# Optimization experiments

Measured on AMD Instinct MI355X. Metric: run time of the kernel, lower is better.

Reference implementation:

```python
import jax, jax.numpy as jnp
import numpy as np

B, T, DIM = 2, 2048, 2048
N_HEAD, N_GROUP = 16, 4
KV_HEAD = N_HEAD // N_GROUP
HEAD_DIM = DIM // N_HEAD


def setup_inputs() -> dict:
    key = jax.random.key(0)
    ks = jax.random.split(key, 7)
    x = jax.random.normal(ks[0], (B, T, DIM), dtype=jnp.float32)
    # rotary tables: last dim = head_dim // 2 (interleaved real/imag pairs)
    pos = jnp.arange(T, dtype=jnp.float32)[:, None]
    inv_freq = 1.0 / (10000.0 ** (jnp.arange(0, HEAD_DIM, 2, dtype=jnp.float32) / HEAD_DIM))
    angles = pos * inv_freq[None, :]  # [T, HEAD_DIM//2]
    freqs_cos = jnp.cos(angles)
    freqs_sin = jnp.sin(angles)
    scale = 0.02
    wq = jax.random.normal(ks[1], (DIM, N_HEAD * HEAD_DIM), dtype=jnp.float32) * scale
    wk = jax.random.normal(ks[2], (DIM, KV_HEAD * HEAD_DIM), dtype=jnp.float32) * scale
    wv = jax.random.normal(ks[3], (DIM, KV_HEAD * HEAD_DIM), dtype=jnp.float32) * scale
    wo = jax.random.normal(ks[4], (N_HEAD * HEAD_DIM, DIM), dtype=jnp.float32) * scale
    return {"x": x, "freqs_cos": freqs_cos, "freqs_sin": freqs_sin,
            "wq": wq, "wk": wk, "wv": wv, "wo": wo}


def _apply_rope(t, cos, sin):
    # t: [B, T, H, D]; interleaved pairs (..., -1, 2) as in torch reference
    tr = t.reshape(*t.shape[:-1], -1, 2)
    r, i = tr[..., 0], tr[..., 1]
    c = cos[None, :, None, :]  # [1, T, 1, D//2]
    s = sin[None, :, None, :]
    out = jnp.stack([r * c - i * s, r * s + i * c], axis=-1)
    return out.reshape(t.shape)


def reference(x, freqs_cos, freqs_sin, wq, wk, wv, wo):
    Bx, Tx, C = x.shape
    xq = (x @ wq).reshape(Bx, Tx, N_HEAD, HEAD_DIM)
    xk = (x @ wk).reshape(Bx, Tx, KV_HEAD, HEAD_DIM)
    xv = (x @ wv).reshape(Bx, Tx, KV_HEAD, HEAD_DIM)
    xq = _apply_rope(xq, freqs_cos, freqs_sin)
    xk = _apply_rope(xk, freqs_cos, freqs_sin)
    # repeat_kv: each kv head repeated n_group times consecutively
    xk = jnp.repeat(xk, N_GROUP, axis=2)  # [B, T, N_HEAD, D]
    xv = jnp.repeat(xv, N_GROUP, axis=2)
    scale = HEAD_DIM ** -0.5
    att = jnp.einsum('bqhd,bkhd->bhqk', xq, xk) * scale
    causal = jnp.tril(jnp.ones((Tx, Tx), dtype=bool))
    att = jnp.where(causal[None, None], att, -jnp.inf)
    att = jax.nn.softmax(att, axis=-1)
    out = jnp.einsum('bhqk,bkhd->bqhd', att, xv).reshape(Bx, Tx, N_HEAD * HEAD_DIM)
    return out @ wo
```

## Files before the change

kernel.cpp:

```cpp
#include <hip/hip_runtime.h>

#define TB 2
#define TT 2048
#define TDIM 2048
#define NHEADS 16
#define KVHEADS 4
#define HD 128

typedef unsigned short u16;
typedef unsigned int u32;
typedef __attribute__((ext_vector_type(8))) short short8;
typedef __attribute__((ext_vector_type(4))) float float4_t;

__device__ __forceinline__ float b2f(u16 u) {
    union { u32 i; float f; } v; v.i = ((u32)u) << 16; return v.f;
}
__device__ __forceinline__ u16 f2b(float f) {
    union { float f; u32 i; } v; v.f = f;
    u32 r = (v.i + 0x7FFFu + ((v.i >> 16) & 1u)) >> 16;
    return (u16)r;
}
__device__ __forceinline__ u32 fbits(float f) {
    union { float f; u32 i; } v; v.f = f; return v.i;
}

__device__ __forceinline__ void gl_lds16(const void* g, void* l) {
    __builtin_amdgcn_global_load_lds((const __attribute__((address_space(1))) void*)g,
                                     (__attribute__((address_space(3))) void*)l, 16, 0, 0);
}

template <bool F32OUT, bool ROPE>
__global__ __launch_bounds__(256, 3)
void gemm_bt(const u16* __restrict__ A, const u16* __restrict__ BT,
             void* __restrict__ Cv, int M, int N, int K,
             const float* __restrict__ fc, const float* __restrict__ fs) {
    __shared__ __align__(16) u16 As[128 * 64];
    __shared__ __align__(16) u16 Bs[128 * 64];
    const int tid  = threadIdx.x;
    const int wave = tid >> 6, lane = tid & 63;
    const int quad = lane >> 4, l16 = lane & 15;
    const int wm = wave >> 1, wn = wave & 1;
    const int row0 = blockIdx.y * 128, col0 = blockIdx.x * 128;

    float4_t acc[4][4];
#pragma unroll
    for (int i = 0; i < 4; i++)
#pragma unroll
        for (int j = 0; j < 4; j++) acc[i][j] = (float4_t){0.f, 0.f, 0.f, 0.f};

    for (int kk = 0; kk < K; kk += 64) {
        __syncthreads();
#pragma unroll
        for (int i = 0; i < 4; i++) {
            int n = i * 256 + wave * 64 + lane;
            int r = n >> 3, c = (n & 7) ^ (r & 7);
            gl_lds16(A  + (size_t)(row0 + r) * K + kk + c * 8, &As[(i * 256 + wave * 64) * 8]);
            gl_lds16(BT + (size_t)(col0 + r) * K + kk + c * 8, &Bs[(i * 256 + wave * 64) * 8]);
        }
        __syncthreads();
#pragma unroll
        for (int ks = 0; ks < 2; ks++) {
            short8 af[4], bf[4];
#pragma unroll
            for (int mt = 0; mt < 4; mt++) {
                int m = wm * 64 + mt * 16 + l16;
                af[mt] = *(const short8*)&As[(m * 8 + ((ks * 4 + quad) ^ (l16 & 7))) * 8];
            }
#pragma unroll
            for (int nt = 0; nt < 4; nt++) {
                int n = wn * 64 + nt * 16 + l16;
                bf[nt] = *(const short8*)&Bs[(n * 8 + ((ks * 4 + quad) ^ (l16 & 7))) * 8];
            }
#pragma unroll
            for (int mt = 0; mt < 4; mt++)
#pragma unroll
                for (int nt = 0; nt < 4; nt++)
                    acc[mt][nt] = __builtin_amdgcn_mfma_f32_16x16x32_bf16(
                        af[mt], bf[nt], acc[mt][nt], 0, 0, 0);
        }
    }
    const bool do_rope = ROPE && (col0 < 2560);
#pragma unroll
    for (int mt = 0; mt < 4; mt++)
#pragma unroll
        for (int nt = 0; nt < 4; nt++)
#pragma unroll
            for (int r = 0; r < 4; r++) {
                int row = row0 + wm * 64 + mt * 16 + quad * 4 + r;
                int col = col0 + wn * 64 + nt * 16 + l16;
                float v = acc[mt][nt][r];
                if (ROPE && do_rope) {
                    float other = __shfl_xor(v, 1, 64);
                    int t = row & (TT - 1);
                    int i0 = (col & (HD - 1)) >> 1;
                    float c = fc[t * 64 + i0], s = fs[t * 64 + i0];
                    v = (col & 1) ? fmaf(v, c, other * s) : fmaf(v, c, -other * s);
                }
                if (F32OUT)
                    ((float*)Cv)[(size_t)row * N + col] = v;
                else
                    ((u16*)Cv)[(size_t)row * N + col] = f2b(v);
            }
}

template <bool F32OUT>
__global__ __launch_bounds__(512, 4)
void gemm_bt8w(const u16* __restrict__ A, const u16* __restrict__ BT,
               void* __restrict__ Cv, int M, int N, int K) {
    __shared__ __align__(16) u16 As[128 * 64];
    __shared__ __align__(16) u16 Bs[128 * 64];
    const int tid  = threadIdx.x;
    const int w    = tid >> 6, lane = tid & 63;
    const int quad = lane >> 4, l16 = lane & 15;
    const int wm = w >> 1, wn = w & 1;
    const int row0 = blockIdx.y * 128, col0 = blockIdx.x * 128;

    float4_t acc[2][4];
#pragma unroll
    for (int i = 0; i < 2; i++)
#pragma unroll
        for (int j = 0; j < 4; j++) acc[i][j] = (float4_t){0.f, 0.f, 0.f, 0.f};

    for (int kk = 0; kk < K; kk += 64) {
        __syncthreads();
#pragma unroll
        for (int j = 0; j < 2; j++) {
            int n = j * 512 + w * 64 + lane;
            int r = n >> 3, c = (n & 7) ^ (r & 7);
            gl_lds16(A  + (size_t)(row0 + r) * K + kk + c * 8, &As[(j * 512 + w * 64) * 8]);
            gl_lds16(BT + (size_t)(col0 + r) * K + kk + c * 8, &Bs[(j * 512 + w * 64) * 8]);
        }
        __syncthreads();
#pragma unroll
        for (int ks = 0; ks < 2; ks++) {
            short8 af[2], bf[4];
#pragma unroll
            for (int mt = 0; mt < 2; mt++) {
                int m = wm * 32 + mt * 16 + l16;
                af[mt] = *(const short8*)&As[(m * 8 + ((ks * 4 + quad) ^ (l16 & 7))) * 8];
            }
#pragma unroll
            for (int nt = 0; nt < 4; nt++) {
                int n = wn * 64 + nt * 16 + l16;
                bf[nt] = *(const short8*)&Bs[(n * 8 + ((ks * 4 + quad) ^ (l16 & 7))) * 8];
            }
#pragma unroll
            for (int mt = 0; mt < 2; mt++)
#pragma unroll
                for (int nt = 0; nt < 4; nt++)
                    acc[mt][nt] = __builtin_amdgcn_mfma_f32_16x16x32_bf16(
                        af[mt], bf[nt], acc[mt][nt], 0, 0, 0);
        }
    }
#pragma unroll
    for (int mt = 0; mt < 2; mt++)
#pragma unroll
        for (int nt = 0; nt < 4; nt++)
#pragma unroll
            for (int r = 0; r < 4; r++) {
                int row = row0 + wm * 32 + mt * 16 + quad * 4 + r;
                int col = col0 + wn * 64 + nt * 16 + l16;
                float v = acc[mt][nt][r];
                if (F32OUT)
                    ((float*)Cv)[(size_t)row * N + col] = v;
                else
                    ((u16*)Cv)[(size_t)row * N + col] = f2b(v);
            }
}

__global__ void prep(const float* __restrict__ x, u16* __restrict__ xb,
                     const float* __restrict__ wq, const float* __restrict__ wk,
                     const float* __restrict__ wv, const float* __restrict__ wo,
                     u16* __restrict__ WT, u16* __restrict__ woT) {
    const int bid = blockIdx.x;
    if (bid < 8192) {
        size_t i = ((size_t)bid * 256 + threadIdx.x) * 4;
        float4 v = *(const float4*)(x + i);
        ushort4 o;
        o.x = f2b(v.x); o.y = f2b(v.y); o.z = f2b(v.z); o.w = f2b(v.w);
        *(ushort4*)(xb + i) = o;
        return;
    }
    const int rem = bid - 8192;
    const int bx = rem % 160;
    const int by = rem / 160;
    const float* in; u16* out; int cols, cx;
    if (bx < 64)      { in = wq; out = WT;                         cols = 2048; cx = bx; }
    else if (bx < 80) { in = wk; out = WT + (size_t)2048 * 2048;   cols = 512;  cx = bx - 64; }
    else if (bx < 96) { in = wv; out = WT + (size_t)2560 * 2048;   cols = 512;  cx = bx - 80; }
    else              { in = wo; out = woT;                        cols = 2048; cx = bx - 96; }
    const int rows = 2048;
    __shared__ u16 tile[32][72];
    const int c0 = cx * 32, r0 = by * 64;
    const int tx = threadIdx.x & 31, ty = threadIdx.x >> 5;
#pragma unroll
    for (int i = 0; i < 8; i++) {
        int r = ty * 8 + i;
        tile[tx][r] = f2b(in[(size_t)(r0 + r) * cols + c0 + tx]);
    }
    __syncthreads();
    const int c = threadIdx.x >> 3, rc = threadIdx.x & 7;
    *(short8*)&out[(size_t)(c0 + c) * rows + r0 + rc * 8] =
        *(const short8*)&tile[c][rc * 8];
}

__global__ void transpose_v(const u16* __restrict__ QKV, u16* __restrict__ Vt) {
    int z = blockIdx.z, b = z >> 2, kv = z & 3;
    const u16* in = QKV + (size_t)b * TT * 3072 + 2560 + kv * HD;
    u16* out = Vt + (size_t)z * HD * TT;
    __shared__ u16 tile[32][72];
    const int t0 = blockIdx.x * 64, d0 = blockIdx.y * 32;
    const int tx = threadIdx.x & 31, ty = threadIdx.x >> 5;
#pragma unroll
    for (int i = 0; i < 8; i++) {
        int r = ty * 8 + i;
        tile[tx][r] = in[(size_t)(t0 + r) * 3072 + d0 + tx];
    }
    __syncthreads();
    const int c = threadIdx.x >> 3, rc = threadIdx.x & 7;
    *(short8*)&out[(size_t)(d0 + c) * TT + t0 + rc * 8] =
        *(const short8*)&tile[c][rc * 8];
}

#define PSTR 72
__global__ __launch_bounds__(256, 3)
void attn(const u16* __restrict__ QKV, const u16* __restrict__ Vt,
          u16* __restrict__ O) {
    const int bid = blockIdx.x;
    const int qb  = 31 - (bid >> 5);
    const int y   = bid & 31;
    const int b   = y >> 4;
    const int h   = y & 15;
    const int kvh = h >> 2;
    const int tid = threadIdx.x, w = tid >> 6, lane = tid & 63;
    const int quad = lane >> 4, l16 = lane & 15;

    __shared__ __align__(16) u16 Ks[64 * 128];
    __shared__ __align__(16) u16 Vs[128 * 64];
    __shared__ __align__(16) u16 Ps[4][16 * PSTR];

    const u16* Kbase = QKV + (size_t)b * TT * 3072 + 2048 + kvh * HD;
    const u16* Vbase = Vt + (size_t)(b * 4 + kvh) * HD * TT;
    const float Cl = 0.12753102474f;

    auto stageK = [&](int kt) {
#pragma unroll
        for (int i = 0; i < 4; i++) {
            int n = i * 256 + w * 64 + lane;
            int r = n >> 4, c = (n & 15) ^ (r & 15);
            gl_lds16(Kbase + (size_t)(kt * 64 + r) * 3072 + c * 8,
                     &Ks[(i * 256 + w * 64) * 8]);
        }
    };
    auto stageV = [&](int kt) {
#pragma unroll
        for (int i = 0; i < 4; i++) {
            int n = i * 256 + w * 64 + lane;
            int d = n >> 3, c = (n & 7) ^ (d & 7);
            gl_lds16(Vbase + (size_t)d * TT + kt * 64 + c * 8,
                     &Vs[(i * 256 + w * 64) * 8]);
        }
    };

    stageK(0);

    short8 qf[4];
    {
        const u16* Qrow = QKV + ((size_t)b * TT + qb * 64 + w * 16 + l16) * 3072
                          + h * HD;
#pragma unroll
        for (int ks = 0; ks < 4; ks++)
            qf[ks] = *(const short8*)(Qrow + ks * 32 + quad * 8);
    }

    float4_t o[8];
#pragma unroll
    for (int i = 0; i < 8; i++) o[i] = (float4_t){0.f, 0.f, 0.f, 0.f};
    float mi = -1e30f, li = 0.f;
    const int qg = qb * 64 + w * 16 + l16;

    for (int kt = 0; kt <= qb; kt++) {
        __syncthreads();
        stageV(kt);

        float4_t st[4];
#pragma unroll
        for (int nt = 0; nt < 4; nt++) st[nt] = (float4_t){0.f, 0.f, 0.f, 0.f};
#pragma unroll
        for (int ks = 0; ks < 4; ks++) {
            short8 af[4];
#pragma unroll
            for (int nt = 0; nt < 4; nt++)
                af[nt] = *(const short8*)&Ks[((nt * 16 + l16) * 16 +
                                             ((ks * 4 + quad) ^ l16)) * 8];
            __builtin_amdgcn_s_setprio(1);
#pragma unroll
            for (int nt = 0; nt < 4; nt++)
                st[nt] = __builtin_amdgcn_mfma_f32_16x16x32_bf16(
                    af[nt], qf[ks], st[nt], 0, 0, 0);
            __builtin_amdgcn_s_setprio(0);
        }

        if (kt == qb) {
#pragma unroll
            for (int nt = 0; nt < 4; nt++)
#pragma unroll
                for (int r = 0; r < 4; r++) {
                    int key = kt * 64 + nt * 16 + quad * 4 + r;
                    if (key > qg) st[nt][r] = -3e38f;
                }
        }
        float pm = -3e38f;
#pragma unroll
        for (int nt = 0; nt < 4; nt++)
#pragma unroll
            for (int r = 0; r < 4; r++) pm = fmaxf(pm, st[nt][r]);
        pm = fmaxf(pm, __shfl_xor(pm, 16, 64));
        pm = fmaxf(pm, __shfl_xor(pm, 32, 64));
        const bool need = !__all(pm - mi <= 62.7f);
        float alpha_v = 1.f;
        if (need) {
            float mnew = fmaxf(mi, pm);
            alpha_v = __builtin_amdgcn_exp2f((mi - mnew) * Cl);
            mi = mnew;
        }
        const float mC = mi * Cl;
        float rs = 0.f;
#pragma unroll
        for (int nt = 0; nt < 4; nt++)
#pragma unroll
            for (int r = 0; r < 4; r++) {
                float e = __builtin_amdgcn_exp2f(fmaf(st[nt][r], Cl, -mC));
                st[nt][r] = e;
                rs += e;
            }
        rs += __shfl_xor(rs, 16, 64);
        rs += __shfl_xor(rs, 32, 64);
        li = li * alpha_v + rs;

#pragma unroll
        for (int nt = 0; nt < 4; nt++) {
            uint2 pk;
            pk.x = __builtin_amdgcn_perm(fbits(st[nt][1]), fbits(st[nt][0]), 0x07060302u);
            pk.y = __builtin_amdgcn_perm(fbits(st[nt][3]), fbits(st[nt][2]), 0x07060302u);
            *(uint2*)&Ps[w][l16 * PSTR + nt * 16 + quad * 4] = pk;
        }
        if (need) {
            float a_o[4];
#pragma unroll
            for (int r = 0; r < 4; r++) a_o[r] = __shfl(alpha_v, quad * 4 + r, 64);
#pragma unroll
            for (int n2 = 0; n2 < 8; n2++)
#pragma unroll
                for (int r = 0; r < 4; r++) o[n2][r] *= a_o[r];
        }

        __syncthreads();
        if (kt < qb) stageK(kt + 1);

#pragma unroll
        for (int ks2 = 0; ks2 < 2; ks2++) {
            short8 ap = *(const short8*)&Ps[w][l16 * PSTR + ks2 * 32 + quad * 8];
            __builtin_amdgcn_s_setprio(1);
#pragma unroll
            for (int n2 = 0; n2 < 8; n2++) {
                short8 bv = *(const short8*)&Vs[((n2 * 16 + l16) * 8 +
                                                ((ks2 * 4 + quad) ^ (l16 & 7))) * 8];
                o[n2] = __builtin_amdgcn_mfma_f32_16x16x32_bf16(ap, bv, o[n2], 0, 0, 0);
            }
            __builtin_amdgcn_s_setprio(0);
        }
    }

    float linv[4];
#pragma unroll
    for (int r = 0; r < 4; r++) linv[r] = 1.0f / __shfl(li, quad * 4 + r, 64);
    u16* Ob2 = O + ((size_t)b * TT + qb * 64 + w * 16) * TDIM + h * HD;
#pragma unroll
    for (int n2 = 0; n2 < 8; n2++)
#pragma unroll
        for (int r = 0; r < 4; r++)
            Ob2[(size_t)(quad * 4 + r) * TDIM + n2 * 16 + l16] =
                f2b(o[n2][r] * linv[r]);
}

extern "C" void kernel_launch(void* const* d_in, const int* in_sizes, int n_in,
                              void* d_out, int out_size, void* d_ws, size_t ws_size,
                              hipStream_t stream) {
    const float* x  = (const float*)d_in[0];
    const float* fc = (const float*)d_in[1];
    const float* fs = (const float*)d_in[2];
    const float* wq = (const float*)d_in[3];
    const float* wk = (const float*)d_in[4];
    const float* wv = (const float*)d_in[5];
    const float* wo = (const float*)d_in[6];
    float* out = (float*)d_out;

    char* ws = (char*)d_ws;
    size_t off = 0;
    auto alloc = [&](size_t bytes) -> void* {
        void* p = ws + off;
        off += (bytes + 255) & ~(size_t)255;
        return p;
    };
    u16* xb  = (u16*)alloc((size_t)4096 * 2048 * 2);
    u16* WT  = (u16*)alloc((size_t)3072 * 2048 * 2);
    u16* woT = (u16*)alloc((size_t)2048 * 2048 * 2);
    u16* QKV = (u16*)alloc((size_t)4096 * 3072 * 2);
    u16* Vtb = (u16*)alloc((size_t)4096 * 512 * 2);
    u16* Ob  = (u16*)alloc((size_t)4096 * 2048 * 2);

    dim3 blk(256);
    prep<<<dim3(8192 + 160 * 32), blk, 0, stream>>>(x, xb, wq, wk, wv, wo, WT, woT);
    gemm_bt<false, true><<<dim3(24, 32), blk, 0, stream>>>(
        xb, WT, QKV, 4096, 3072, 2048, fc, fs);
    transpose_v<<<dim3(32, 4, 8), blk, 0, stream>>>(QKV, Vtb);
    attn<<<dim3(1024), blk, 0, stream>>>(QKV, Vtb, Ob);
    gemm_bt8w<true><<<dim3(16, 32), dim3(512), 0, stream>>>(
        Ob, woT, out, 4096, 2048, 2048);
}
```

Before: 289.6 us.

## Rewrite QKV GEMM as 256x256 double-buffered 8-wave pipelined kernel

Replaces the 128x128, 4-wave QKV projection GEMM with a 256x256-tile, 8-wave kernel that double-buffers LDS. Global-to-LDS loads for later K tiles are interleaved with quarter-tile MFMA phases, and each phase is fenced by barriers, explicit vmcnt waits and raised wave priority during MFMA. The intent is to hide load latency and increase operand reuse per block. In exchange the grid shrinks to 192 blocks, which may underfill the GPU, and the kernel uses 128KB of LDS per block.

```diff
diff --git a/kernel.cpp b/kernel.cpp
--- a/kernel.cpp
+++ b/kernel.cpp
@@ -29,66 +29,140 @@
                                      (__attribute__((address_space(3))) void*)l, 16, 0, 0);
 }
 
+#define MM16(mh, nh)                                                          \
+    do {                                                                      \
+        asm volatile("s_waitcnt lgkmcnt(0)");                                 \
+        __builtin_amdgcn_s_setprio(1);                                        \
+        _Pragma("unroll") for (int ks = 0; ks < 2; ks++)                      \
+        _Pragma("unroll") for (int mq = 0; mq < 4; mq++)                      \
+        _Pragma("unroll") for (int nq = 0; nq < 2; nq++)                      \
+            acc[(mh) * 4 + mq][(nh) * 2 + nq] =                               \
+                __builtin_amdgcn_mfma_f32_16x16x32_bf16(                      \
+                    af[mq][ks], bf[nq][ks],                                   \
+                    acc[(mh) * 4 + mq][(nh) * 2 + nq], 0, 0, 0);              \
+        __builtin_amdgcn_s_setprio(0);                                        \
+    } while (0)
+
+#define BAR() __builtin_amdgcn_s_barrier()
+
 template <bool F32OUT, bool ROPE>
-__global__ __launch_bounds__(256, 3)
-void gemm_bt(const u16* __restrict__ A, const u16* __restrict__ BT,
-             void* __restrict__ Cv, int M, int N, int K,
-             const float* __restrict__ fc, const float* __restrict__ fs) {
-    __shared__ __align__(16) u16 As[128 * 64];
-    __shared__ __align__(16) u16 Bs[128 * 64];
+__global__ __launch_bounds__(512, 2)
+void gemm_bt8(const u16* __restrict__ A, const u16* __restrict__ BT,
+              void* __restrict__ Cv, int M, int N, int K,
+              const float* __restrict__ fc, const float* __restrict__ fs) {
+    __shared__ __align__(16) u16 As[2][256 * 64];
+    __shared__ __align__(16) u16 Bs[2][256 * 64];
     const int tid  = threadIdx.x;
-    const int wave = tid >> 6, lane = tid & 63;
+    const int w    = tid >> 6, lane = tid & 63;
     const int quad = lane >> 4, l16 = lane & 15;
-    const int wm = wave >> 1, wn = wave & 1;
-    const int row0 = blockIdx.y * 128, col0 = blockIdx.x * 128;
-
-    float4_t acc[4][4];
-#pragma unroll
-    for (int i = 0; i < 4; i++)
+    const int wm = w >> 2, wn = w & 3;
+    const int row0 = blockIdx.y * 256, col0 = blockIdx.x * 256;
+    const int nkt = K >> 6, nit = nkt >> 1;
+
+    float4_t acc[8][4];
+#pragma unroll
+    for (int i = 0; i < 8; i++)
 #pragma unroll
         for (int j = 0; j < 4; j++) acc[i][j] = (float4_t){0.f, 0.f, 0.f, 0.f};
 
-    for (int kk = 0; kk < K; kk += 64) {
-        __syncthreads();
-#pragma unroll
-        for (int i = 0; i < 4; i++) {
-            int n = i * 256 + wave * 64 + lane;
+    auto stA = [&](int half, int T) {
+        if (T >= nkt) return;
+#pragma unroll
+        for (int j = 0; j < 2; j++) {
+            int n = j * 512 + tid;
             int r = n >> 3, c = (n & 7) ^ (r & 7);
-            gl_lds16(A  + (size_t)(row0 + r) * K + kk + c * 8, &As[(i * 256 + wave * 64) * 8]);
-            gl_lds16(BT + (size_t)(col0 + r) * K + kk + c * 8, &Bs[(i * 256 + wave * 64) * 8]);
-        }
-        __syncthreads();
-#pragma unroll
-        for (int ks = 0; ks < 2; ks++) {
-            short8 af[4], bf[4];
-#pragma unroll
-            for (int mt = 0; mt < 4; mt++) {
-                int m = wm * 64 + mt * 16 + l16;
-                af[mt] = *(const short8*)&As[(m * 8 + ((ks * 4 + quad) ^ (l16 & 7))) * 8];
-            }
-#pragma unroll
-            for (int nt = 0; nt < 4; nt++) {
-                int n = wn * 64 + nt * 16 + l16;
-                bf[nt] = *(const short8*)&Bs[(n * 8 + ((ks * 4 + quad) ^ (l16 & 7))) * 8];
-            }
-#pragma unroll
-            for (int mt = 0; mt < 4; mt++)
-#pragma unroll
-                for (int nt = 0; nt < 4; nt++)
-                    acc[mt][nt] = __builtin_amdgcn_mfma_f32_16x16x32_bf16(
-                        af[mt], bf[nt], acc[mt][nt], 0, 0, 0);
-        }
-    }
+            gl_lds16(A + (size_t)(row0 + half * 128 + r) * K + T * 64 + c * 8,
+                     &As[T & 1][(half * 1024 + j * 512 + w * 64) * 8]);
+        }
+    };
+    auto stB = [&](int half, int T) {
+        if (T >= nkt) return;
+#pragma unroll
+        for (int j = 0; j < 2; j++) {
+            int n = j * 512 + tid;
+            int r = n >> 3, c = (n & 7) ^ (r & 7);
+            gl_lds16(BT + (size_t)(col0 + half * 128 + r) * K + T * 64 + c * 8,
+                     &Bs[T & 1][(half * 1024 + j * 512 + w * 64) * 8]);
+        }
+    };
+
+    short8 af[4][2], bf[2][2];
+    auto ldA = [&](int mh, int p) {
+#pragma unroll
+        for (int mq = 0; mq < 4; mq++) {
+            int row = mh * 128 + wm * 64 + mq * 16 + l16;
+#pragma unroll
+            for (int ks = 0; ks < 2; ks++)
+                af[mq][ks] = *(const short8*)
+                    &As[p][(row * 8 + ((ks * 4 + quad) ^ (row & 7))) * 8];
+        }
+    };
+    auto ldB = [&](int nh, int p) {
+#pragma unroll
+        for (int nq = 0; nq < 2; nq++) {
+            int row = nh * 128 + wn * 32 + nq * 16 + l16;
+#pragma unroll
+            for (int ks = 0; ks < 2; ks++)
+                bf[nq][ks] = *(const short8*)
+                    &Bs[p][(row * 8 + ((ks * 4 + quad) ^ (row & 7))) * 8];
+        }
+    };
+
+    stA(0, 0); stB(0, 0); stB(1, 0); stA(1, 0);
+    stA(0, 1); stB(1, 1); stA(1, 1);
+    asm volatile("s_waitcnt vmcnt(6)");
+    BAR();
+
+    for (int i = 0; i < nit; i++) {
+        const int T0 = i * 2;
+        const bool last = (i == nit - 1);
+        ldA(0, 0); ldB(0, 0);
+        stB(0, T0 + 1);
+        BAR(); MM16(0, 0); BAR();
+
+        ldB(1, 0);
+        stA(0, T0 + 2);
+        BAR(); MM16(0, 1); BAR();
+
+        ldA(1, 0);
+        stB(1, T0 + 2);
+        BAR(); MM16(1, 1); BAR();
+
+        ldB(0, 0);
+        stA(1, T0 + 2);
+        if (last) asm volatile("s_waitcnt vmcnt(0)");
+        else      asm volatile("s_waitcnt vmcnt(6)");
+        BAR(); MM16(1, 0); BAR();
+
+        ldA(0, 1); ldB(0, 1);
+        stB(0, T0 + 2);
+        BAR(); MM16(0, 0); BAR();
+
+        ldB(1, 1);
+        stA(0, T0 + 3);
+        BAR(); MM16(0, 1); BAR();
+
+        ldA(1, 1);
+        stB(1, T0 + 3);
+        BAR(); MM16(1, 1); BAR();
+
+        ldB(0, 1);
+        stA(1, T0 + 3);
+        if (last) asm volatile("s_waitcnt vmcnt(0)");
+        else      asm volatile("s_waitcnt vmcnt(6)");
+        BAR(); MM16(1, 0); BAR();
+    }
+
     const bool do_rope = ROPE && (col0 < 2560);
 #pragma unroll
-    for (int mt = 0; mt < 4; mt++)
-#pragma unroll
-        for (int nt = 0; nt < 4; nt++)
+    for (int ai = 0; ai < 8; ai++)
+#pragma unroll
+        for (int bj = 0; bj < 4; bj++)
 #pragma unroll
             for (int r = 0; r < 4; r++) {
-                int row = row0 + wm * 64 + mt * 16 + quad * 4 + r;
-                int col = col0 + wn * 64 + nt * 16 + l16;
-                float v = acc[mt][nt][r];
+                int row = row0 + (ai >> 2) * 128 + wm * 64 + (ai & 3) * 16 + quad * 4 + r;
+                int col = col0 + (bj >> 1) * 128 + wn * 32 + (bj & 1) * 16 + l16;
+                float v = acc[ai][bj][r];
                 if (ROPE && do_rope) {
                     float other = __shfl_xor(v, 1, 64);
                     int t = row & (TT - 1);
@@ -412,7 +486,7 @@
 
     dim3 blk(256);
     prep<<<dim3(8192 + 160 * 32), blk, 0, stream>>>(x, xb, wq, wk, wv, wo, WT, woT);
-    gemm_bt<false, true><<<dim3(24, 32), blk, 0, stream>>>(
+    gemm_bt8<false, true><<<dim3(12, 16), dim3(512), 0, stream>>>(
         xb, WT, QKV, 4096, 3072, 2048, fc, fs);
     transpose_v<<<dim3(32, 4, 8), blk, 0, stream>>>(QKV, Vtb);
     attn<<<dim3(1024), blk, 0, stream>>>(QKV, Vtb, Ob);
```

Result: slower. 305.4 us (+5.4%).
